# Kernel optimization log

Hardware: AMD Instinct MI355X
Metric: run time of the kernel (lower is better)

## Reference

```python
import jax, jax.numpy as jnp
import numpy as np

N, D, H, OUT, L = 4096, 127, 128, 3, 2
SIM_THRESH = 0.9
BN_EPS = 1e-5


def setup_inputs() -> dict:
    key = jax.random.key(0)
    ks = jax.random.split(key, 10)
    s = 1.0 / np.sqrt(H)
    x_now = jax.random.normal(ks[0], (N, D), dtype=jnp.float32)
    sat_type = jax.random.randint(ks[1], (N,), 0, 6, dtype=jnp.int64)
    # SAGEConv per layer: lin_l (neighbor aggr, with bias) and lin_r (root, no bias)
    Wl = jax.random.normal(ks[2], (L, H, H), dtype=jnp.float32) * s
    bl = jnp.zeros((L, H), dtype=jnp.float32)
    Wr = jax.random.normal(ks[3], (L, H, H), dtype=jnp.float32) * s
    gamma = jnp.ones((H,), dtype=jnp.float32)
    beta = jnp.zeros((H,), dtype=jnp.float32)
    Wo = jax.random.normal(ks[4], (OUT, H), dtype=jnp.float32) * s
    bo = jnp.zeros((OUT,), dtype=jnp.float32)
    return {"x_now": x_now, "sat_type": sat_type, "Wl": Wl, "bl": bl,
            "Wr": Wr, "gamma": gamma, "beta": beta, "Wo": Wo, "bo": bo}


def _forward(x_now, sat_type, Wl, bl, Wr, gamma, beta, Wo, bo):
    n = x_now.shape[0]
    # build_graph, h_prev=None branch: ppr = x_now[:, 0]
    x = jnp.concatenate([x_now[:, :1], x_now], axis=1)  # [N, H] with H = D+1
    # pairwise cosine similarity on first 4 features (F.normalize, eps=1e-12)
    f = x[:, :4]
    fn = f / jnp.maximum(jnp.linalg.norm(f, axis=1, keepdims=True), 1e-12)
    cos_sim = fn @ fn.T  # [N, N]
    same = sat_type[:, None] == sat_type[None, :]
    mask = (same | (cos_sim > SIM_THRESH)) & ~jnp.eye(n, dtype=bool)
    A = mask.astype(x.dtype)  # symmetric adjacency (dense form of edge list)
    deg = jnp.maximum(A.sum(axis=1, keepdims=True), 1.0)  # mean-aggr denom; isolated -> 0
    h = x
    for l in range(L):  # SAGEConv: lin_l(mean_j x_j) + lin_r(x_i), then ReLU
        m = (A @ h) / deg
        h = jax.nn.relu(m @ Wl[l].T + bl[l] + h @ Wr[l].T)
    # BatchNorm over nodes (training-mode batch stats, biased variance)
    mu = h.mean(axis=0)
    var = h.var(axis=0)
    h = (h - mu) / jnp.sqrt(var + BN_EPS) * gamma + beta
    out = h @ Wo.T + bo
    return h, out


def reference(x_now, sat_type, Wl, bl, Wr, gamma, beta, Wo, bo):
    return _forward(x_now, sat_type, Wl, bl, Wr, gamma, beta, Wo, bo)
```

## Files before the change

### kernel.cpp

```cpp
#include <hip/hip_runtime.h>
#include <hip/hip_bf16.h>
#include <math.h>

#define NN 4096
#define DD 127
#define HH 128
#define OUTD 3
#define NTYPES 6
#define SIM_THRESH 0.9f
#define BN_EPS 1e-5f
#define MROW 4
#define NREP 8
#define LMAXH 256

typedef unsigned short ushortT;
typedef __attribute__((ext_vector_type(8))) short short8;
typedef __attribute__((ext_vector_type(4))) float f32x4;

static __device__ inline ushortT f2bf(float f) {
    unsigned u = __float_as_uint(f);
    unsigned r = (u + 0x7fffu + ((u >> 16) & 1u)) >> 16;
    return (ushortT)r;
}

__global__ __launch_bounds__(256) void prep(
    const float* __restrict__ x_now, const int* __restrict__ sat,
    const float* __restrict__ Wl, const float* __restrict__ Wr,
    ushortT* __restrict__ Wbf, float* __restrict__ x,
    ushortT* __restrict__ xbf, float4* __restrict__ fn,
    int* __restrict__ cnt, float* __restrict__ S0rep)
{
    int t = threadIdx.x;
    if (blockIdx.x < 8) {
        int baseidx = blockIdx.x * 8192;
        #pragma unroll
        for (int it = 0; it < 32; ++it) {
            int idx = baseidx + it * 256 + t;
            float v = (idx < 32768) ? Wl[idx] : Wr[idx - 32768];
            Wbf[idx] = f2bf(v);
        }
        return;
    }

    int sb = blockIdx.x - 8;
    int base = sb * 16;
    int rep = sb & (NREP - 1);
    __shared__ int stypes[16];
    int myti = -1;
    if (t < 16) {
        int row = base + t;
        int ti = sat[row]; ti = min(max(ti, 0), NTYPES - 1);
        stypes[t] = ti; myti = ti;
        const float* rp = x_now + (size_t)row * DD;
        float f0 = rp[0], f2 = rp[1], f3 = rp[2];
        float nrm = fmaxf(sqrtf(2.f * f0 * f0 + f2 * f2 + f3 * f3), 1e-12f);
        float inv = 1.f / nrm;
        fn[row] = make_float4(f0 * inv, f0 * inv, f2 * inv, f3 * inv);
    }
    #pragma unroll
    for (int it = 0; it < 8; ++it) {
        int lin = it * 256 + t;
        int rl = lin >> 7, col = lin & 127;
        int row = base + rl;
        const float* rp = x_now + (size_t)row * DD;
        float v = (col == 0) ? rp[0] : rp[col - 1];
        x[(size_t)row * HH + col] = v;
        xbf[(size_t)row * HH + col] = f2bf(v);
    }
    __syncthreads();
    if (t < 64) {
        #pragma unroll
        for (int tt = 0; tt < NTYPES; ++tt) {
            unsigned long long m = __ballot(myti == tt);
            if (t == 0) {
                int c = __popcll(m);
                if (c) atomicAdd(&cnt[rep * NTYPES + tt], c);
            }
        }
    }
    if (t < 128) {
        float acc[NTYPES] = {0.f, 0.f, 0.f, 0.f, 0.f, 0.f};
        for (int r = 0; r < 16; ++r) {
            float v = x[(size_t)(base + r) * HH + t];
            int tt = stypes[r];
            #pragma unroll
            for (int q = 0; q < NTYPES; ++q) acc[q] += (tt == q) ? v : 0.f;
        }
        #pragma unroll
        for (int q = 0; q < NTYPES; ++q)
            atomicAdd(&S0rep[(rep * NTYPES + q) * HH + t], acc[q]);
    }
}

__global__ __launch_bounds__(256) void build_mask(
    const float4* __restrict__ fn, const int* __restrict__ sat,
    const int* __restrict__ cnt, unsigned* __restrict__ mask,
    float* __restrict__ deg)
{
    int i0 = blockIdx.x * MROW;
    int t = threadIdx.x;
    int w = t & 127;
    int half = t >> 7;
    float4 fi[MROW];
    int ti[MROW];
    #pragma unroll
    for (int r = 0; r < MROW; ++r) {
        fi[r] = fn[i0 + r];
        int tt = sat[i0 + r];
        ti[r] = min(max(tt, 0), NTYPES - 1);
    }
    unsigned word[MROW] = {0, 0, 0, 0};
    int bbase = half * 16;
    for (int bb = 0; bb < 16; ++bb) {
        int b = bbase + bb;
        int j = b * 128 + w;
        float4 fj = fn[j];
        int tj = sat[j];
        #pragma unroll
        for (int r = 0; r < MROW; ++r) {
            float dot = fi[r].x * fj.x + fi[r].y * fj.y
                      + fi[r].z * fj.z + fi[r].w * fj.w;
            if (tj != ti[r] && dot > SIM_THRESH) word[r] |= (1u << b);
        }
    }
    __shared__ unsigned wpart[MROW][128];
    if (half == 1) {
        #pragma unroll
        for (int r = 0; r < MROW; ++r) wpart[r][w] = word[r];
    }
    __syncthreads();
    __shared__ int wt[2][MROW];
    if (half == 0) {
        int pcs[MROW];
        #pragma unroll
        for (int r = 0; r < MROW; ++r) {
            unsigned full = word[r] | wpart[r][w];
            mask[(size_t)(i0 + r) * 128 + w] = full;
            pcs[r] = __popc(full);
        }
        int lane = w & 63, wv2 = w >> 6;
        for (int s = 32; s; s >>= 1) {
            #pragma unroll
            for (int r = 0; r < MROW; ++r) pcs[r] += __shfl_down(pcs[r], s);
        }
        if (lane == 0) {
            #pragma unroll
            for (int r = 0; r < MROW; ++r) wt[wv2][r] = pcs[r];
        }
    }
    __syncthreads();
    if (t < MROW) {
        int r = t;
        int ctot = 0;
        #pragma unroll
        for (int rr = 0; rr < NREP; ++rr) ctot += cnt[rr * NTYPES + ti[r]];
        float d = (float)(ctot - 1 + wt[0][r] + wt[1][r]);
        deg[i0 + r] = fmaxf(d, 1.0f);
    }
}

__global__ __launch_bounds__(256, 8) void gather_kernel(
    const float* __restrict__ h, const ushortT* __restrict__ hbf,
    const unsigned* __restrict__ mask, const float* __restrict__ deg,
    const float* __restrict__ S, const int* __restrict__ sat,
    ushortT* __restrict__ mbf)
{
    int t = threadIdx.x;
    int wv = t >> 6;
    int lane = t & 63;
    int r  = wv >> 1;
    int hf = wv & 1;
    int i0 = blockIdx.x * 2;
    int i = i0 + r;

    __shared__ ushortT list[4][LMAXH];
    __shared__ __align__(16) float hs[2][HH];
    __shared__ __align__(16) float part[4][HH];
    __shared__ int tarr[2];

    if (t < 2) {
        int tt = sat[i0 + t];
        tarr[t] = min(max(tt, 0), NTYPES - 1);
    }

    int widx = hf * 64 + lane;
    unsigned word = mask[(size_t)i * 128 + widx];
    int pc = __popc(word);
    int x = pc;
    for (int s = 1; s < 64; s <<= 1) {
        int v = __shfl_up(x, s);
        if (lane >= s) x += v;
    }
    int ncnt = __shfl(x, 63);
    int ofs = x - pc;
    unsigned ww = word;
    while (ww) {
        int b = __ffs(ww) - 1; ww &= ww - 1;
        list[wv][ofs++] = (ushortT)(b * 128 + widx);
    }
    if (hf == 0)
        ((float2*)hs[r])[lane] = ((const float2*)(h + (size_t)i * HH))[lane];

    int q = lane >> 4;
    int c = lane & 15;
    const uint4* __restrict__ hb4 = (const uint4*)hbf;
    float acc[8] = {0.f, 0.f, 0.f, 0.f, 0.f, 0.f, 0.f, 0.f};
#define BFACC(vv)                                                         \
    {                                                                     \
        acc[0] += __uint_as_float((vv).x << 16);                          \
        acc[1] += __uint_as_float((vv).x & 0xffff0000u);                  \
        acc[2] += __uint_as_float((vv).y << 16);                          \
        acc[3] += __uint_as_float((vv).y & 0xffff0000u);                  \
        acc[4] += __uint_as_float((vv).z << 16);                          \
        acc[5] += __uint_as_float((vv).z & 0xffff0000u);                  \
        acc[6] += __uint_as_float((vv).w << 16);                          \
        acc[7] += __uint_as_float((vv).w & 0xffff0000u);                  \
    }
    int g = 0;
    for (; g + 24 <= ncnt; g += 24) {
        int j0 = list[wv][g + q];
        int j1 = list[wv][g + 4 + q];
        int j2 = list[wv][g + 8 + q];
        int j3 = list[wv][g + 12 + q];
        int j4 = list[wv][g + 16 + q];
        int j5 = list[wv][g + 20 + q];
        uint4 v0 = hb4[j0 * 16 + c];
        uint4 v1 = hb4[j1 * 16 + c];
        uint4 v2 = hb4[j2 * 16 + c];
        uint4 v3 = hb4[j3 * 16 + c];
        uint4 v4 = hb4[j4 * 16 + c];
        uint4 v5 = hb4[j5 * 16 + c];
        BFACC(v0); BFACC(v1); BFACC(v2); BFACC(v3); BFACC(v4); BFACC(v5);
    }
    for (; g + 4 <= ncnt; g += 4) {
        int j0 = list[wv][g + q];
        uint4 v0 = hb4[j0 * 16 + c];
        BFACC(v0);
    }
    if (q < ncnt - g) {
        int j0 = list[wv][g + q];
        uint4 v0 = hb4[j0 * 16 + c];
        BFACC(v0);
    }
#undef BFACC
    #pragma unroll
    for (int d = 0; d < 8; ++d) {
        acc[d] += __shfl_down(acc[d], 32);
        acc[d] += __shfl_down(acc[d], 16);
    }
    if (lane < 16) {
        float4 p0 = {acc[0], acc[1], acc[2], acc[3]};
        float4 p1 = {acc[4], acc[5], acc[6], acc[7]};
        ((float4*)part[wv])[c * 2] = p0;
        ((float4*)part[wv])[c * 2 + 1] = p1;
    }
    __syncthreads();

    if (hf == 0 && lane < 32) {
        int cc = lane;
        float4 p0 = ((const float4*)part[wv])[cc];
        float4 p1 = ((const float4*)part[wv + 1])[cc];
        int ti = tarr[r];
        float rdeg = 1.f / deg[i];
        float4 hv = ((const float4*)hs[r])[cc];
        float4 Sv = {0.f, 0.f, 0.f, 0.f};
        #pragma unroll
        for (int rr = 0; rr < NREP; ++rr) {
            float4 sv = ((const float4*)S)[(rr * NTYPES + ti) * 32 + cc];
            Sv.x += sv.x; Sv.y += sv.y; Sv.z += sv.z; Sv.w += sv.w;
        }
        float4 m;
        m.x = (Sv.x - hv.x + p0.x + p1.x) * rdeg;
        m.y = (Sv.y - hv.y + p0.y + p1.y) * rdeg;
        m.z = (Sv.z - hv.z + p0.z + p1.z) * rdeg;
        m.w = (Sv.w - hv.w + p0.w + p1.w) * rdeg;
        ushort4 mb;
        mb.x = f2bf(m.x); mb.y = f2bf(m.y);
        mb.z = f2bf(m.z); mb.w = f2bf(m.w);
        ((ushort4*)(mbf + (size_t)i * HH))[cc] = mb;
    }
}

template <int MODE>
__global__ __launch_bounds__(256) void gemm_kernel(
    const ushortT* __restrict__ mbf, const ushortT* __restrict__ hbf,
    const ushortT* __restrict__ Wlbf, const ushortT* __restrict__ Wrbf,
    const float* __restrict__ bl, const int* __restrict__ sat,
    float* __restrict__ hout, ushortT* __restrict__ houtbf,
    float* __restrict__ acc0, float* __restrict__ acc1)
{
    int t = threadIdx.x;
    int wv = t >> 6, lane = t & 63;
    int p = lane & 15, q = lane >> 4;
    int i0 = blockIdx.x * 16;

    __shared__ float sh[16][129];
    __shared__ int stypes[16];
    if (t < 16) {
        int tt = sat[i0 + t];
        stypes[t] = min(max(tt, 0), NTYPES - 1);
    }

    const ushortT* arow_m = mbf + (size_t)(i0 + p) * HH + q * 8;
    const ushortT* arow_h = hbf + (size_t)(i0 + p) * HH + q * 8;
    short8 am[4], ah[4];
    #pragma unroll
    for (int s = 0; s < 4; ++s) {
        am[s] = *(const short8*)(arow_m + s * 32);
        ah[s] = *(const short8*)(arow_h + s * 32);
    }

    #pragma unroll
    for (int nt = 0; nt < 2; ++nt) {
        int n0 = (wv * 2 + nt) * 16;
        const ushortT* brow_l = Wlbf + (size_t)(n0 + p) * HH + q * 8;
        const ushortT* brow_r = Wrbf + (size_t)(n0 + p) * HH + q * 8;
        f32x4 acc = {0.f, 0.f, 0.f, 0.f};
        #pragma unroll
        for (int s = 0; s < 4; ++s) {
            short8 b = *(const short8*)(brow_l + s * 32);
            acc = __builtin_amdgcn_mfma_f32_16x16x32_bf16(am[s], b, acc, 0, 0, 0);
        }
        #pragma unroll
        for (int s = 0; s < 4; ++s) {
            short8 b = *(const short8*)(brow_r + s * 32);
            acc = __builtin_amdgcn_mfma_f32_16x16x32_bf16(ah[s], b, acc, 0, 0, 0);
        }
        int o = n0 + p;
        float bv = bl[o];
        #pragma unroll
        for (int rg = 0; rg < 4; ++rg) {
            float v = fmaxf(acc[rg] + bv, 0.f);
            sh[q * 4 + rg][o] = v;
        }
    }
    __syncthreads();

    #pragma unroll
    for (int e = 0; e < 8; ++e) {
        int lin = e * 256 + t;
        int rr = lin >> 7, cc = lin & 127;
        float v = sh[rr][cc];
        hout[(size_t)i0 * HH + lin] = v;
        if (MODE == 1) houtbf[(size_t)i0 * HH + lin] = f2bf(v);
    }
    int rep = blockIdx.x & (NREP - 1);
    if (t < HH) {
        if (MODE == 1) {
            float accq[NTYPES] = {0.f, 0.f, 0.f, 0.f, 0.f, 0.f};
            for (int r = 0; r < 16; ++r) {
                float v = sh[r][t];
                int tt = stypes[r];
                #pragma unroll
                for (int qq = 0; qq < NTYPES; ++qq)
                    accq[qq] += (tt == qq) ? v : 0.f;
            }
            #pragma unroll
            for (int qq = 0; qq < NTYPES; ++qq)
                atomicAdd(&acc0[(rep * NTYPES + qq) * HH + t], accq[qq]);
        } else {
            float s = 0.f, s2 = 0.f;
            for (int r = 0; r < 16; ++r) {
                float v = sh[r][t];
                s += v; s2 += v * v;
            }
            atomicAdd(&acc0[rep * HH + t], s);
            atomicAdd(&acc1[rep * HH + t], s2);
        }
    }
}

__global__ __launch_bounds__(256) void finalize(
    const float* __restrict__ h, const float* __restrict__ musum8,
    const float* __restrict__ varsum8, const float* __restrict__ gamma,
    const float* __restrict__ beta, const float* __restrict__ Wo,
    const float* __restrict__ bo, float* __restrict__ out_h,
    float* __restrict__ out_o)
{
    int t = threadIdx.x;
    int wv = t >> 6;
    int lane = t & 63;
    int i = blockIdx.x * 4 + wv;

    float2 mus = {0.f, 0.f}, vas = {0.f, 0.f};
    #pragma unroll
    for (int r = 0; r < NREP; ++r) {
        float2 a = ((const float2*)(musum8 + r * HH))[lane];
        float2 b = ((const float2*)(varsum8 + r * HH))[lane];
        mus.x += a.x; mus.y += a.y;
        vas.x += b.x; vas.y += b.y;
    }
    float2 ga  = ((const float2*)gamma)[lane];
    float2 be  = ((const float2*)beta)[lane];
    float mu0 = mus.x * (1.f / NN), mu1 = mus.y * (1.f / NN);
    float v0 = vas.x * (1.f / NN) - mu0 * mu0;
    float v1 = vas.y * (1.f / NN) - mu1 * mu1;
    float sc0 = ga.x / sqrtf(v0 + BN_EPS), sc1 = ga.y / sqrtf(v1 + BN_EPS);
    float sh0 = be.x - mu0 * sc0, sh1 = be.y - mu1 * sc1;

    float2 hv = ((const float2*)(h + (size_t)i * HH))[lane];
    float2 hb;
    hb.x = hv.x * sc0 + sh0;
    hb.y = hv.y * sc1 + sh1;
    ((float2*)(out_h + (size_t)i * HH))[lane] = hb;

    float2 w0 = ((const float2*)Wo)[lane];
    float2 w1 = ((const float2*)(Wo + HH))[lane];
    float2 w2 = ((const float2*)(Wo + 2 * HH))[lane];
    float p0 = hb.x * w0.x + hb.y * w0.y;
    float p1 = hb.x * w1.x + hb.y * w1.y;
    float p2 = hb.x * w2.x + hb.y * w2.y;
    for (int s = 32; s; s >>= 1) {
        p0 += __shfl_down(p0, s);
        p1 += __shfl_down(p1, s);
        p2 += __shfl_down(p2, s);
    }
    if (lane == 0) {
        out_o[(size_t)i * OUTD + 0] = p0 + bo[0];
        out_o[(size_t)i * OUTD + 1] = p1 + bo[1];
        out_o[(size_t)i * OUTD + 2] = p2 + bo[2];
    }
}

extern "C" void kernel_launch(void* const* d_in, const int* in_sizes, int n_in,
                              void* d_out, int out_size, void* d_ws, size_t ws_size,
                              hipStream_t stream)
{
    (void)in_sizes; (void)n_in; (void)out_size; (void)ws_size;
    const float* x_now = (const float*)d_in[0];
    const int*   sat   = (const int*)d_in[1];
    const float* Wl    = (const float*)d_in[2];
    const float* bl    = (const float*)d_in[3];
    const float* Wr    = (const float*)d_in[4];
    const float* gamma = (const float*)d_in[5];
    const float* beta  = (const float*)d_in[6];
    const float* Wo    = (const float*)d_in[7];
    const float* bo    = (const float*)d_in[8];

    float* ws = (float*)d_ws;
    float* x0 = ws;
    float* h1 = x0 + (size_t)NN * HH;
    float* h2 = h1 + (size_t)NN * HH;
    ushortT* Wbf  = (ushortT*)(h2 + (size_t)NN * HH);
    ushortT* x0bf = Wbf + 65536;
    ushortT* h1bf = x0bf + (size_t)NN * HH;
    ushortT* mbf  = h1bf + (size_t)NN * HH;
    float4* fn = (float4*)(mbf + (size_t)NN * HH);
    unsigned* mask = (unsigned*)((float*)fn + 4 * NN);
    float* deg = (float*)(mask + (size_t)NN * 128);
    int*   cnt   = (int*)(deg + NN);
    float* S0rep = (float*)(cnt + 64);
    float* S1rep = S0rep + NREP * NTYPES * HH;
    float* mu8   = S1rep + NREP * NTYPES * HH;
    float* var8  = mu8 + NREP * HH;

    size_t zero_bytes = (64 + 2 * NREP * NTYPES * HH + 2 * NREP * HH)
                        * sizeof(float);
    hipMemsetAsync(cnt, 0, zero_bytes, stream);

    prep<<<264, 256, 0, stream>>>(x_now, sat, Wl, Wr, Wbf, x0, x0bf, fn, cnt,
                                  S0rep);
    build_mask<<<NN / MROW, 256, 0, stream>>>(fn, sat, cnt, mask, deg);

    gather_kernel<<<NN / 2, 256, 0, stream>>>(x0, x0bf, mask, deg, S0rep, sat,
                                              mbf);
    gemm_kernel<1><<<NN / 16, 256, 0, stream>>>(
        mbf, x0bf, Wbf, Wbf + 32768, bl, sat, h1, h1bf, S1rep, nullptr);

    gather_kernel<<<NN / 2, 256, 0, stream>>>(h1, h1bf, mask, deg, S1rep, sat,
                                              mbf);
    gemm_kernel<2><<<NN / 16, 256, 0, stream>>>(
        mbf, h1bf, Wbf + 16384, Wbf + 49152, bl + HH, sat, h2, nullptr,
        mu8, var8);

    finalize<<<NN / 4, 256, 0, stream>>>(h2, mu8, var8, gamma, beta, Wo, bo,
                                         (float*)d_out, (float*)d_out + (size_t)NN * HH);
}
```

Measured before the change: 136.9 us.

## Fuse mask build with first gather and BN finalize into layer-2 GEMM

Merges the adjacency-mask construction with the first-layer neighbor gather, and folds BatchNorm plus the output projection into the second GEMM kernel using a device-wide atomic barrier. This cuts the launch count from seven to five. It also drops the fp32 copies of x0, h1 and h2 and reads the bf16 versions instead, which reduces global traffic. The grid barrier assumes all 256 blocks are co-resident or it can deadlock. Reading the self term from bf16 changes rounding slightly.

Result: slower. 151.8 us (+10.9%).

```diff
diff --git a/kernel.cpp b/kernel.cpp
--- a/kernel.cpp
+++ b/kernel.cpp
@@ -1,5 +1,4 @@
 #include <hip/hip_runtime.h>
-#include <hip/hip_bf16.h>
 #include <math.h>
 
 #define NN 4096
@@ -11,6 +10,7 @@
 #define BN_EPS 1e-5f
 #define MROW 4
 #define NREP 8
+#define LMAX 384
 #define LMAXH 256
 
 typedef unsigned short ushortT;
@@ -22,13 +22,26 @@
     unsigned r = (u + 0x7fffu + ((u >> 16) & 1u)) >> 16;
     return (ushortT)r;
 }
+static __device__ inline float bflo(unsigned w) { return __uint_as_float(w << 16); }
+static __device__ inline float bfhi(unsigned w) { return __uint_as_float(w & 0xffff0000u); }
+
+#define BFACC(vv)                                                         \
+    {                                                                     \
+        acc[0] += __uint_as_float((vv).x << 16);                          \
+        acc[1] += __uint_as_float((vv).x & 0xffff0000u);                  \
+        acc[2] += __uint_as_float((vv).y << 16);                          \
+        acc[3] += __uint_as_float((vv).y & 0xffff0000u);                  \
+        acc[4] += __uint_as_float((vv).z << 16);                          \
+        acc[5] += __uint_as_float((vv).z & 0xffff0000u);                  \
+        acc[6] += __uint_as_float((vv).w << 16);                          \
+        acc[7] += __uint_as_float((vv).w & 0xffff0000u);                  \
+    }
 
 __global__ __launch_bounds__(256) void prep(
     const float* __restrict__ x_now, const int* __restrict__ sat,
     const float* __restrict__ Wl, const float* __restrict__ Wr,
-    ushortT* __restrict__ Wbf, float* __restrict__ x,
-    ushortT* __restrict__ xbf, float4* __restrict__ fn,
-    int* __restrict__ cnt, float* __restrict__ S0rep)
+    ushortT* __restrict__ Wbf, ushortT* __restrict__ xbf,
+    float4* __restrict__ fn, int* __restrict__ cnt, float* __restrict__ S0rep)
 {
     int t = threadIdx.x;
     if (blockIdx.x < 8) {
@@ -46,6 +59,7 @@
     int base = sb * 16;
     int rep = sb & (NREP - 1);
     __shared__ int stypes[16];
+    __shared__ float xs[16][HH];
     int myti = -1;
     if (t < 16) {
         int row = base + t;
@@ -64,7 +78,7 @@
         int row = base + rl;
         const float* rp = x_now + (size_t)row * DD;
         float v = (col == 0) ? rp[0] : rp[col - 1];
-        x[(size_t)row * HH + col] = v;
+        xs[rl][col] = v;
         xbf[(size_t)row * HH + col] = f2bf(v);
     }
     __syncthreads();
@@ -81,7 +95,7 @@
     if (t < 128) {
         float acc[NTYPES] = {0.f, 0.f, 0.f, 0.f, 0.f, 0.f};
         for (int r = 0; r < 16; ++r) {
-            float v = x[(size_t)(base + r) * HH + t];
+            float v = xs[r][t];
             int tt = stypes[r];
             #pragma unroll
             for (int q = 0; q < NTYPES; ++q) acc[q] += (tt == q) ? v : 0.f;
@@ -92,15 +106,23 @@
     }
 }
 
-__global__ __launch_bounds__(256) void build_mask(
+__global__ __launch_bounds__(256) void maskgather(
     const float4* __restrict__ fn, const int* __restrict__ sat,
-    const int* __restrict__ cnt, unsigned* __restrict__ mask,
-    float* __restrict__ deg)
+    const int* __restrict__ cnt, const float* __restrict__ S,
+    const ushortT* __restrict__ hbf, unsigned* __restrict__ mask,
+    float* __restrict__ deg, ushortT* __restrict__ mbf)
 {
     int i0 = blockIdx.x * MROW;
     int t = threadIdx.x;
     int w = t & 127;
     int half = t >> 7;
+
+    __shared__ unsigned wbuf[MROW][HH];
+    __shared__ ushortT list[MROW][LMAX];
+    __shared__ float sdeg[MROW];
+    __shared__ int stypes[MROW];
+    __shared__ int wt[2][MROW];
+
     float4 fi[MROW];
     int ti[MROW];
     #pragma unroll
@@ -123,18 +145,17 @@
             if (tj != ti[r] && dot > SIM_THRESH) word[r] |= (1u << b);
         }
     }
-    __shared__ unsigned wpart[MROW][128];
     if (half == 1) {
         #pragma unroll
-        for (int r = 0; r < MROW; ++r) wpart[r][w] = word[r];
-    }
-    __syncthreads();
-    __shared__ int wt[2][MROW];
+        for (int r = 0; r < MROW; ++r) wbuf[r][w] = word[r];
+    }
+    __syncthreads();
     if (half == 0) {
         int pcs[MROW];
         #pragma unroll
         for (int r = 0; r < MROW; ++r) {
-            unsigned full = word[r] | wpart[r][w];
+            unsigned full = word[r] | wbuf[r][w];
+            wbuf[r][w] = full;
             mask[(size_t)(i0 + r) * 128 + w] = full;
             pcs[r] = __popc(full);
         }
@@ -155,67 +176,40 @@
         #pragma unroll
         for (int rr = 0; rr < NREP; ++rr) ctot += cnt[rr * NTYPES + ti[r]];
         float d = (float)(ctot - 1 + wt[0][r] + wt[1][r]);
-        deg[i0 + r] = fmaxf(d, 1.0f);
-    }
-}
-
-__global__ __launch_bounds__(256, 8) void gather_kernel(
-    const float* __restrict__ h, const ushortT* __restrict__ hbf,
-    const unsigned* __restrict__ mask, const float* __restrict__ deg,
-    const float* __restrict__ S, const int* __restrict__ sat,
-    ushortT* __restrict__ mbf)
-{
-    int t = threadIdx.x;
-    int wv = t >> 6;
-    int lane = t & 63;
-    int r  = wv >> 1;
-    int hf = wv & 1;
-    int i0 = blockIdx.x * 2;
-    int i = i0 + r;
-
-    __shared__ ushortT list[4][LMAXH];
-    __shared__ __align__(16) float hs[2][HH];
-    __shared__ __align__(16) float part[4][HH];
-    __shared__ int tarr[2];
-
-    if (t < 2) {
-        int tt = sat[i0 + t];
-        tarr[t] = min(max(tt, 0), NTYPES - 1);
-    }
-
-    int widx = hf * 64 + lane;
-    unsigned word = mask[(size_t)i * 128 + widx];
-    int pc = __popc(word);
-    int x = pc;
+        d = fmaxf(d, 1.0f);
+        sdeg[r] = d;
+        deg[i0 + r] = d;
+        stypes[r] = ti[r];
+    }
+    __syncthreads();
+
+    int wv = t >> 6, lane = t & 63;
+    int i = i0 + wv;
+    unsigned w0 = wbuf[wv][lane];
+    unsigned w1 = wbuf[wv][lane + 64];
+    int pc0 = __popc(w0), pc1 = __popc(w1);
+    int x = pc0 + pc1;
     for (int s = 1; s < 64; s <<= 1) {
         int v = __shfl_up(x, s);
         if (lane >= s) x += v;
     }
     int ncnt = __shfl(x, 63);
-    int ofs = x - pc;
-    unsigned ww = word;
+    int ofs = x - pc0 - pc1;
+    unsigned ww = w0;
     while (ww) {
         int b = __ffs(ww) - 1; ww &= ww - 1;
-        list[wv][ofs++] = (ushortT)(b * 128 + widx);
-    }
-    if (hf == 0)
-        ((float2*)hs[r])[lane] = ((const float2*)(h + (size_t)i * HH))[lane];
+        list[wv][ofs++] = (ushortT)(b * 128 + lane);
+    }
+    ww = w1;
+    while (ww) {
+        int b = __ffs(ww) - 1; ww &= ww - 1;
+        list[wv][ofs++] = (ushortT)(b * 128 + lane + 64);
+    }
 
     int q = lane >> 4;
     int c = lane & 15;
     const uint4* __restrict__ hb4 = (const uint4*)hbf;
     float acc[8] = {0.f, 0.f, 0.f, 0.f, 0.f, 0.f, 0.f, 0.f};
-#define BFACC(vv)                                                         \
-    {                                                                     \
-        acc[0] += __uint_as_float((vv).x << 16);                          \
-        acc[1] += __uint_as_float((vv).x & 0xffff0000u);                  \
-        acc[2] += __uint_as_float((vv).y << 16);                          \
-        acc[3] += __uint_as_float((vv).y & 0xffff0000u);                  \
-        acc[4] += __uint_as_float((vv).z << 16);                          \
-        acc[5] += __uint_as_float((vv).z & 0xffff0000u);                  \
-        acc[6] += __uint_as_float((vv).w << 16);                          \
-        acc[7] += __uint_as_float((vv).w & 0xffff0000u);                  \
-    }
     int g = 0;
     for (; g + 24 <= ncnt; g += 24) {
         int j0 = list[wv][g + q];
@@ -242,7 +236,107 @@
         uint4 v0 = hb4[j0 * 16 + c];
         BFACC(v0);
     }
-#undef BFACC
+    #pragma unroll
+    for (int d = 0; d < 8; ++d) {
+        acc[d] += __shfl_down(acc[d], 32);
+        acc[d] += __shfl_down(acc[d], 16);
+    }
+    if (lane < 16) {
+        int tti = stypes[wv];
+        float rdeg = 1.f / sdeg[wv];
+        float4 Sv0 = {0.f, 0.f, 0.f, 0.f}, Sv1 = {0.f, 0.f, 0.f, 0.f};
+        #pragma unroll
+        for (int rr = 0; rr < NREP; ++rr) {
+            float4 a = ((const float4*)S)[(rr * NTYPES + tti) * 32 + c * 2];
+            float4 b = ((const float4*)S)[(rr * NTYPES + tti) * 32 + c * 2 + 1];
+            Sv0.x += a.x; Sv0.y += a.y; Sv0.z += a.z; Sv0.w += a.w;
+            Sv1.x += b.x; Sv1.y += b.y; Sv1.z += b.z; Sv1.w += b.w;
+        }
+        uint4 hw = ((const uint4*)(hbf + (size_t)i * HH))[c];
+        float m0 = (Sv0.x - bflo(hw.x) + acc[0]) * rdeg;
+        float m1 = (Sv0.y - bfhi(hw.x) + acc[1]) * rdeg;
+        float m2 = (Sv0.z - bflo(hw.y) + acc[2]) * rdeg;
+        float m3 = (Sv0.w - bfhi(hw.y) + acc[3]) * rdeg;
+        float m4 = (Sv1.x - bflo(hw.z) + acc[4]) * rdeg;
+        float m5 = (Sv1.y - bfhi(hw.z) + acc[5]) * rdeg;
+        float m6 = (Sv1.z - bflo(hw.w) + acc[6]) * rdeg;
+        float m7 = (Sv1.w - bfhi(hw.w) + acc[7]) * rdeg;
+        ushort4 a4, b4;
+        a4.x = f2bf(m0); a4.y = f2bf(m1); a4.z = f2bf(m2); a4.w = f2bf(m3);
+        b4.x = f2bf(m4); b4.y = f2bf(m5); b4.z = f2bf(m6); b4.w = f2bf(m7);
+        ((ushort4*)(mbf + (size_t)i * HH))[c * 2] = a4;
+        ((ushort4*)(mbf + (size_t)i * HH))[c * 2 + 1] = b4;
+    }
+}
+
+__global__ __launch_bounds__(256, 8) void gather2(
+    const ushortT* __restrict__ hbf, const unsigned* __restrict__ mask,
+    const float* __restrict__ deg, const float* __restrict__ S,
+    const int* __restrict__ sat, ushortT* __restrict__ mbf)
+{
+    int t = threadIdx.x;
+    int wv = t >> 6;
+    int lane = t & 63;
+    int r  = wv >> 1;
+    int hf = wv & 1;
+    int i0 = blockIdx.x * 2;
+    int i = i0 + r;
+
+    __shared__ ushortT list[4][LMAXH];
+    __shared__ __align__(16) float part[4][HH];
+    __shared__ int tarr[2];
+
+    if (t < 2) {
+        int tt = sat[i0 + t];
+        tarr[t] = min(max(tt, 0), NTYPES - 1);
+    }
+
+    int widx = hf * 64 + lane;
+    unsigned word = mask[(size_t)i * 128 + widx];
+    int pc = __popc(word);
+    int x = pc;
+    for (int s = 1; s < 64; s <<= 1) {
+        int v = __shfl_up(x, s);
+        if (lane >= s) x += v;
+    }
+    int ncnt = __shfl(x, 63);
+    int ofs = x - pc;
+    unsigned ww = word;
+    while (ww) {
+        int b = __ffs(ww) - 1; ww &= ww - 1;
+        list[wv][ofs++] = (ushortT)(b * 128 + widx);
+    }
+
+    int q = lane >> 4;
+    int c = lane & 15;
+    const uint4* __restrict__ hb4 = (const uint4*)hbf;
+    float acc[8] = {0.f, 0.f, 0.f, 0.f, 0.f, 0.f, 0.f, 0.f};
+    int g = 0;
+    for (; g + 24 <= ncnt; g += 24) {
+        int j0 = list[wv][g + q];
+        int j1 = list[wv][g + 4 + q];
+        int j2 = list[wv][g + 8 + q];
+        int j3 = list[wv][g + 12 + q];
+        int j4 = list[wv][g + 16 + q];
+        int j5 = list[wv][g + 20 + q];
+        uint4 v0 = hb4[j0 * 16 + c];
+        uint4 v1 = hb4[j1 * 16 + c];
+        uint4 v2 = hb4[j2 * 16 + c];
+        uint4 v3 = hb4[j3 * 16 + c];
+        uint4 v4 = hb4[j4 * 16 + c];
+        uint4 v5 = hb4[j5 * 16 + c];
+        BFACC(v0); BFACC(v1); BFACC(v2); BFACC(v3); BFACC(v4); BFACC(v5);
+    }
+    for (; g + 4 <= ncnt; g += 4) {
+        int j0 = list[wv][g + q];
+        uint4 v0 = hb4[j0 * 16 + c];
+        BFACC(v0);
+    }
+    if (q < ncnt - g) {
+        int j0 = list[wv][g + q];
+        uint4 v0 = hb4[j0 * 16 + c];
+        BFACC(v0);
+    }
     #pragma unroll
     for (int d = 0; d < 8; ++d) {
         acc[d] += __shfl_down(acc[d], 32);
@@ -262,7 +356,8 @@
         float4 p1 = ((const float4*)part[wv + 1])[cc];
         int ti = tarr[r];
         float rdeg = 1.f / deg[i];
-        float4 hv = ((const float4*)hs[r])[cc];
+        uint2 hw = ((const uint2*)(hbf + (size_t)i * HH))[cc];
+        float4 hv = {bflo(hw.x), bfhi(hw.x), bflo(hw.y), bfhi(hw.y)};
         float4 Sv = {0.f, 0.f, 0.f, 0.f};
         #pragma unroll
         for (int rr = 0; rr < NREP; ++rr) {
@@ -281,13 +376,11 @@
     }
 }
 
-template <int MODE>
-__global__ __launch_bounds__(256) void gemm_kernel(
+__global__ __launch_bounds__(256) void gemm_l1(
     const ushortT* __restrict__ mbf, const ushortT* __restrict__ hbf,
     const ushortT* __restrict__ Wlbf, const ushortT* __restrict__ Wrbf,
     const float* __restrict__ bl, const int* __restrict__ sat,
-    float* __restrict__ hout, ushortT* __restrict__ houtbf,
-    float* __restrict__ acc0, float* __restrict__ acc1)
+    ushortT* __restrict__ houtbf, float* __restrict__ acc0)
 {
     int t = threadIdx.x;
     int wv = t >> 6, lane = t & 63;
@@ -340,85 +433,146 @@
     for (int e = 0; e < 8; ++e) {
         int lin = e * 256 + t;
         int rr = lin >> 7, cc = lin & 127;
-        float v = sh[rr][cc];
-        hout[(size_t)i0 * HH + lin] = v;
-        if (MODE == 1) houtbf[(size_t)i0 * HH + lin] = f2bf(v);
+        houtbf[(size_t)i0 * HH + lin] = f2bf(sh[rr][cc]);
     }
     int rep = blockIdx.x & (NREP - 1);
     if (t < HH) {
-        if (MODE == 1) {
-            float accq[NTYPES] = {0.f, 0.f, 0.f, 0.f, 0.f, 0.f};
-            for (int r = 0; r < 16; ++r) {
-                float v = sh[r][t];
-                int tt = stypes[r];
-                #pragma unroll
-                for (int qq = 0; qq < NTYPES; ++qq)
-                    accq[qq] += (tt == qq) ? v : 0.f;
-            }
+        float accq[NTYPES] = {0.f, 0.f, 0.f, 0.f, 0.f, 0.f};
+        for (int r = 0; r < 16; ++r) {
+            float v = sh[r][t];
+            int tt = stypes[r];
             #pragma unroll
             for (int qq = 0; qq < NTYPES; ++qq)
-                atomicAdd(&acc0[(rep * NTYPES + qq) * HH + t], accq[qq]);
-        } else {
-            float s = 0.f, s2 = 0.f;
-            for (int r = 0; r < 16; ++r) {
-                float v = sh[r][t];
-                s += v; s2 += v * v;
-            }
-            atomicAdd(&acc0[rep * HH + t], s);
-            atomicAdd(&acc1[rep * HH + t], s2);
-        }
+                accq[qq] += (tt == qq) ? v : 0.f;
+        }
+        #pragma unroll
+        for (int qq = 0; qq < NTYPES; ++qq)
+            atomicAdd(&acc0[(rep * NTYPES + qq) * HH + t], accq[qq]);
     }
 }
 
-__global__ __launch_bounds__(256) void finalize(
-    const float* __restrict__ h, const float* __restrict__ musum8,
-    const float* __restrict__ varsum8, const float* __restrict__ gamma,
-    const float* __restrict__ beta, const float* __restrict__ Wo,
-    const float* __restrict__ bo, float* __restrict__ out_h,
-    float* __restrict__ out_o)
+__global__ __launch_bounds__(256) void gemm_l2_final(
+    const ushortT* __restrict__ mbf, const ushortT* __restrict__ hbf,
+    const ushortT* __restrict__ Wlbf, const ushortT* __restrict__ Wrbf,
+    const float* __restrict__ bl,
+    float* __restrict__ musum, float* __restrict__ varsum,
+    int* __restrict__ done,
+    const float* __restrict__ gamma, const float* __restrict__ beta,
+    const float* __restrict__ Wo, const float* __restrict__ bo,
+    float* __restrict__ out_h, float* __restrict__ out_o)
 {
     int t = threadIdx.x;
-    int wv = t >> 6;
-    int lane = t & 63;
-    int i = blockIdx.x * 4 + wv;
-
-    float2 mus = {0.f, 0.f}, vas = {0.f, 0.f};
-    #pragma unroll
-    for (int r = 0; r < NREP; ++r) {
-        float2 a = ((const float2*)(musum8 + r * HH))[lane];
-        float2 b = ((const float2*)(varsum8 + r * HH))[lane];
-        mus.x += a.x; mus.y += a.y;
-        vas.x += b.x; vas.y += b.y;
-    }
-    float2 ga  = ((const float2*)gamma)[lane];
-    float2 be  = ((const float2*)beta)[lane];
-    float mu0 = mus.x * (1.f / NN), mu1 = mus.y * (1.f / NN);
-    float v0 = vas.x * (1.f / NN) - mu0 * mu0;
-    float v1 = vas.y * (1.f / NN) - mu1 * mu1;
-    float sc0 = ga.x / sqrtf(v0 + BN_EPS), sc1 = ga.y / sqrtf(v1 + BN_EPS);
-    float sh0 = be.x - mu0 * sc0, sh1 = be.y - mu1 * sc1;
-
-    float2 hv = ((const float2*)(h + (size_t)i * HH))[lane];
-    float2 hb;
-    hb.x = hv.x * sc0 + sh0;
-    hb.y = hv.y * sc1 + sh1;
-    ((float2*)(out_h + (size_t)i * HH))[lane] = hb;
+    int wv = t >> 6, lane = t & 63;
+    int p = lane & 15, q = lane >> 4;
+    int i0 = blockIdx.x * 16;
+
+    __shared__ float sh[16][129];
+    __shared__ float ssc[HH], ssh[HH];
+
+    const ushortT* arow_m = mbf + (size_t)(i0 + p) * HH + q * 8;
+    const ushortT* arow_h = hbf + (size_t)(i0 + p) * HH + q * 8;
+    short8 am[4], ah[4];
+    #pragma unroll
+    for (int s = 0; s < 4; ++s) {
+        am[s] = *(const short8*)(arow_m + s * 32);
+        ah[s] = *(const short8*)(arow_h + s * 32);
+    }
+
+    #pragma unroll
+    for (int nt = 0; nt < 2; ++nt) {
+        int n0 = (wv * 2 + nt) * 16;
+        const ushortT* brow_l = Wlbf + (size_t)(n0 + p) * HH + q * 8;
+        const ushortT* brow_r = Wrbf + (size_t)(n0 + p) * HH + q * 8;
+        f32x4 acc = {0.f, 0.f, 0.f, 0.f};
+        #pragma unroll
+        for (int s = 0; s < 4; ++s) {
+            short8 b = *(const short8*)(brow_l + s * 32);
+            acc = __builtin_amdgcn_mfma_f32_16x16x32_bf16(am[s], b, acc, 0, 0, 0);
+        }
+        #pragma unroll
+        for (int s = 0; s < 4; ++s) {
+            short8 b = *(const short8*)(brow_r + s * 32);
+            acc = __builtin_amdgcn_mfma_f32_16x16x32_bf16(ah[s], b, acc, 0, 0, 0);
+        }
+        int o = n0 + p;
+        float bv = bl[o];
+        #pragma unroll
+        for (int rg = 0; rg < 4; ++rg) {
+            float v = fmaxf(acc[rg] + bv, 0.f);
+            sh[q * 4 + rg][o] = v;
+        }
+    }
+    __syncthreads();
+
+    int rep = blockIdx.x & (NREP - 1);
+    if (t < HH) {
+        float s = 0.f, s2 = 0.f;
+        for (int r = 0; r < 16; ++r) {
+            float v = sh[r][t];
+            s += v; s2 += v * v;
+        }
+        atomicAdd(&musum[rep * HH + t], s);
+        atomicAdd(&varsum[rep * HH + t], s2);
+    }
+    __syncthreads();
+    __threadfence();
+    if (t == 0) {
+        __hip_atomic_fetch_add(done, 1, __ATOMIC_ACQ_REL, __HIP_MEMORY_SCOPE_AGENT);
+        while (__hip_atomic_load(done, __ATOMIC_ACQUIRE,
+                                 __HIP_MEMORY_SCOPE_AGENT) < NN / 16) {
+            __builtin_amdgcn_s_sleep(2);
+        }
+    }
+    __syncthreads();
+
+    if (t < HH) {
+        float ms = 0.f, vs = 0.f;
+        #pragma unroll
+        for (int r = 0; r < NREP; ++r) {
+            ms += __hip_atomic_load(&musum[r * HH + t], __ATOMIC_RELAXED,
+                                    __HIP_MEMORY_SCOPE_AGENT);
+            vs += __hip_atomic_load(&varsum[r * HH + t], __ATOMIC_RELAXED,
+                                    __HIP_MEMORY_SCOPE_AGENT);
+        }
+        float mu = ms * (1.f / NN);
+        float va = vs * (1.f / NN) - mu * mu;
+        float sc = gamma[t] / sqrtf(va + BN_EPS);
+        ssc[t] = sc;
+        ssh[t] = beta[t] - mu * sc;
+    }
+    __syncthreads();
+
+    #pragma unroll
+    for (int e = 0; e < 8; ++e) {
+        int lin = e * 256 + t;
+        int rr = lin >> 7, cc = lin & 127;
+        float v = sh[rr][cc] * ssc[cc] + ssh[cc];
+        sh[rr][cc] = v;
+        out_h[(size_t)i0 * HH + lin] = v;
+    }
+    __syncthreads();
 
     float2 w0 = ((const float2*)Wo)[lane];
     float2 w1 = ((const float2*)(Wo + HH))[lane];
     float2 w2 = ((const float2*)(Wo + 2 * HH))[lane];
-    float p0 = hb.x * w0.x + hb.y * w0.y;
-    float p1 = hb.x * w1.x + hb.y * w1.y;
-    float p2 = hb.x * w2.x + hb.y * w2.y;
-    for (int s = 32; s; s >>= 1) {
-        p0 += __shfl_down(p0, s);
-        p1 += __shfl_down(p1, s);
-        p2 += __shfl_down(p2, s);
-    }
-    if (lane == 0) {
-        out_o[(size_t)i * OUTD + 0] = p0 + bo[0];
-        out_o[(size_t)i * OUTD + 1] = p1 + bo[1];
-        out_o[(size_t)i * OUTD + 2] = p2 + bo[2];
+    #pragma unroll
+    for (int rr = 0; rr < 4; ++rr) {
+        int row = wv * 4 + rr;
+        float a = sh[row][lane * 2];
+        float b = sh[row][lane * 2 + 1];
+        float p0 = a * w0.x + b * w0.y;
+        float p1 = a * w1.x + b * w1.y;
+        float p2 = a * w2.x + b * w2.y;
+        for (int s = 32; s; s >>= 1) {
+            p0 += __shfl_down(p0, s);
+            p1 += __shfl_down(p1, s);
+            p2 += __shfl_down(p2, s);
+        }
+        if (lane == 0) {
+            out_o[(size_t)(i0 + row) * OUTD + 0] = p0 + bo[0];
+            out_o[(size_t)(i0 + row) * OUTD + 1] = p1 + bo[1];
+            out_o[(size_t)(i0 + row) * OUTD + 2] = p2 + bo[2];
+        }
     }
 }
 
@@ -437,11 +591,7 @@
     const float* Wo    = (const float*)d_in[7];
     const float* bo    = (const float*)d_in[8];
 
-    float* ws = (float*)d_ws;
-    float* x0 = ws;
-    float* h1 = x0 + (size_t)NN * HH;
-    float* h2 = h1 + (size_t)NN * HH;
-    ushortT* Wbf  = (ushortT*)(h2 + (size_t)NN * HH);
+    ushortT* Wbf  = (ushortT*)d_ws;
     ushortT* x0bf = Wbf + 65536;
     ushortT* h1bf = x0bf + (size_t)NN * HH;
     ushortT* mbf  = h1bf + (size_t)NN * HH;
@@ -453,26 +603,20 @@
     float* S1rep = S0rep + NREP * NTYPES * HH;
     float* mu8   = S1rep + NREP * NTYPES * HH;
     float* var8  = mu8 + NREP * HH;
-
-    size_t zero_bytes = (64 + 2 * NREP * NTYPES * HH + 2 * NREP * HH)
+    int*   done  = (int*)(var8 + NREP * HH);
+
+    size_t zero_bytes = (64 + 2 * NREP * NTYPES * HH + 2 * NREP * HH + 16)
                         * sizeof(float);
     hipMemsetAsync(cnt, 0, zero_bytes, stream);
 
-    prep<<<264, 256, 0, stream>>>(x_now, sat, Wl, Wr, Wbf, x0, x0bf, fn, cnt,
+    prep<<<264, 256, 0, stream>>>(x_now, sat, Wl, Wr, Wbf, x0bf, fn, cnt,
                                   S0rep);
-    build_mask<<<NN / MROW, 256, 0, stream>>>(fn, sat, cnt, mask, deg);
-
-    gather_kernel<<<NN / 2, 256, 0, stream>>>(x0, x0bf, mask, deg, S0rep, sat,
-                                              mbf);
-    gemm_kernel<1><<<NN / 16, 256, 0, stream>>>(
-        mbf, x0bf, Wbf, Wbf + 32768, bl, sat, h1, h1bf, S1rep, nullptr);
-
-    gather_kernel<<<NN / 2, 256, 0, stream>>>(h1, h1bf, mask, deg, S1rep, sat,
-                                              mbf);
-    gemm_kernel<2><<<NN / 16, 256, 0, stream>>>(
-        mbf, h1bf, Wbf + 16384, Wbf + 49152, bl + HH, sat, h2, nullptr,
-        mu8, var8);
-
-    finalize<<<NN / 4, 256, 0, stream>>>(h2, mu8, var8, gamma, beta, Wo, bo,
-                                         (float*)d_out, (float*)d_out + (size_t)NN * HH);
+    maskgather<<<NN / MROW, 256, 0, stream>>>(fn, sat, cnt, S0rep, x0bf,
+                                              mask, deg, mbf);
+    gemm_l1<<<NN / 16, 256, 0, stream>>>(mbf, x0bf, Wbf, Wbf + 32768, bl, sat,
+                                         h1bf, S1rep);
+    gather2<<<NN / 2, 256, 0, stream>>>(h1bf, mask, deg, S1rep, sat, mbf);
+    gemm_l2_final<<<NN / 16, 256, 0, stream>>>(
+        mbf, h1bf, Wbf + 16384, Wbf + 49152, bl + HH, mu8, var8, done,
+        gamma, beta, Wo, bo, (float*)d_out, (float*)d_out + (size_t)NN * HH);
 }
```
